# Performance work log

Measured on AMD Instinct MI355X. Metric: run time of the kernel, lower is better.

## Reference

```python
import jax, jax.numpy as jnp
import numpy as np

N_NODES = 30000
N_EDGES = 480000
C = 32          # channel multiplicity of hidden irreps (32x0e + 32x1o)
L = 3           # graph_net_steps
H = 64          # radial MLP hidden width
NB = 8          # num radial basis functions
NS = 5          # num_species
R_MAX = 4.0
AVG_NEIGH = 16.0
N_PATHS = 5     # tensor-product paths per layer


def setup_inputs() -> dict:
    key = jax.random.key(0)
    ks = jax.random.split(key, 16)

    def w(k, shape, fan_in):
        return jax.random.normal(k, shape, jnp.float32) / np.sqrt(fan_in)

    return {
        "vectors": jax.random.normal(ks[0], (N_EDGES, 3), jnp.float32),
        "node_specie": jax.random.randint(ks[1], (N_NODES,), 0, NS),
        "senders": jax.random.randint(ks[2], (N_EDGES,), 0, N_NODES),
        "receivers": jax.random.randint(ks[3], (N_EDGES,), 0, N_NODES),
        "emb": jax.random.normal(ks[4], (NS, C), jnp.float32),
        "w_rad1": w(ks[5], (L, NB, H), NB),
        "w_rad2": w(ks[6], (L, H, H), H),
        "w_rad_out": w(ks[7], (L, H, N_PATHS * C), H),
        "w_lin_s": w(ks[8], (L, 2 * C, 2 * C), 2 * C),
        "w_lin_v": w(ks[9], (L, 3 * C, C), 3 * C),
        "w_sc_s": w(ks[10], (L, NS, C, 2 * C), C),
        "w_sc_v": w(ks[11], (L, NS, C, C), C),
        "w_out1": w(ks[12], (C, 16), C),
        "w_out2": w(ks[13], (16, 1), 16),
    }


def _envelope(x, p=6):
    # smooth polynomial cutoff, = 1 at x=0, = 0 (with zero derivs) at x=1
    u = (1.0 - (p + 1) * (p + 2) / 2 * x**p + p * (p + 2) * x**(p + 1)
         - p * (p + 1) / 2 * x**(p + 2))
    return jnp.where(x < 1.0, u, 0.0)


def _radial_basis(lengths):
    # bessel radial basis [E, NB] with smooth cutoff envelope
    n = jnp.arange(1, NB + 1, dtype=jnp.float32)
    x = lengths / R_MAX
    b = np.sqrt(2.0 / R_MAX) * jnp.sin(n * np.pi * x[:, None]) \
        / jnp.maximum(lengths, 1e-9)[:, None]
    return b * _envelope(x)[:, None]


def reference(vectors, node_specie, senders, receivers, emb, w_rad1, w_rad2,
              w_rad_out, w_lin_s, w_lin_v, w_sc_s, w_sc_v, w_out1, w_out2):
    vectors = vectors / R_MAX                       # as in original __call__
    lengths = jnp.linalg.norm(vectors, axis=-1)
    nhat = vectors / jnp.maximum(lengths, 1e-9)[:, None]   # unit edge vectors
    rb = _radial_basis(lengths)                     # [E, NB]

    s = emb[node_specie]                            # [N, C] scalars (0e)
    v = jnp.zeros((s.shape[0], C, 3), s.dtype)      # [N, C, 3] vectors (1o)

    for l in range(L):
        # radial MLP -> per-path, per-channel edge weights
        h = jax.nn.silu(rb @ w_rad1[l])
        h = jax.nn.silu(h @ w_rad2[l])
        wgt = (h @ w_rad_out[l]).reshape(-1, N_PATHS, C)        # [E, 5, C]

        s_u = s[senders]                                         # [E, C]
        v_u = v[senders]                                         # [E, C, 3]
        ndv = jnp.einsum('ed,ecd->ec', nhat, v_u)                # <n, v>

        # CG tensor-product message paths with spherical harmonics of n
        p0 = wgt[:, 0] * s_u                                     # 0e x Y0 -> 0e
        p1 = wgt[:, 1] * ndv                                     # 1o x Y1 -> 0e
        p2 = wgt[:, 2][:, :, None] * (s_u[:, :, None] * nhat[:, None, :])  # 0e x Y1 -> 1o
        p3 = wgt[:, 3][:, :, None] * v_u                         # 1o x Y0 -> 1o
        p4 = wgt[:, 4][:, :, None] * (nhat[:, None, :] * ndv[:, :, None] - v_u / 3.0)  # 1o x Y2 -> 1o

        agg_s = jax.ops.segment_sum(jnp.concatenate([p0, p1], 1), receivers,
                                    num_segments=N_NODES) / AVG_NEIGH      # [N, 2C]
        agg_v = jax.ops.segment_sum(jnp.concatenate([p2, p3, p4], 1), receivers,
                                    num_segments=N_NODES) / AVG_NEIGH      # [N, 3C, 3]

        sg = agg_s @ w_lin_s[l]                                  # [N, 2C]: C feats + C gates
        vn = jnp.einsum('npd,pc->ncd', agg_v, w_lin_v[l])        # [N, C, 3]
        # self-connection: per-species linear (== tp with species one-hot)
        sg = sg + jnp.einsum('nc,nck->nk', s, w_sc_s[l][node_specie])
        vn = vn + jnp.einsum('ncd,nck->nkd', v, w_sc_v[l][node_specie])

        s_new, gates = jnp.split(sg, 2, axis=1)
        s = jax.nn.silu(s_new)                                   # even activation
        v = jax.nn.silu(gates)[:, :, None] * vn                  # gated 1o

    e = (s @ w_out1) @ w_out2            # Linear '16x0e' -> Linear '0e'
    return e[:, 0]                        # per-node energy [N]
```

## Files before the change

kernel.cpp:

```cpp
#include <hip/hip_runtime.h>
#include <math.h>

#define NNODES 30000
#define NEDGES 480000
#define NC 32
#define NL 3
#define NH 64
#define NBASIS 8
#define NSPEC 5
#define INV_AVG 0.0625f

typedef _Float16 half2v __attribute__((ext_vector_type(2)));
typedef _Float16 half4v __attribute__((ext_vector_type(4)));
typedef _Float16 half8v __attribute__((ext_vector_type(8)));
typedef float    float4v __attribute__((ext_vector_type(4)));
typedef unsigned int uint32;

__device__ __forceinline__ float silu_f(float x) {
    return x / (1.f + __expf(-x));
}
__device__ __forceinline__ float rdlane(float v, int k) {
    return __uint_as_float(__builtin_amdgcn_readlane(__float_as_uint(v), k));
}


__global__ void geom_kernel(const float* __restrict__ vec,
                            float* __restrict__ nhat4,
                            float* __restrict__ rb) {
    int e = blockIdx.x * blockDim.x + threadIdx.x;
    if (e >= NEDGES) return;
    float vx = vec[3*e+0] * 0.25f;
    float vy = vec[3*e+1] * 0.25f;
    float vz = vec[3*e+2] * 0.25f;
    float len = sqrtf(vx*vx + vy*vy + vz*vz);
    float inv = 1.f / fmaxf(len, 1e-9f);
    float4 nh = make_float4(vx*inv, vy*inv, vz*inv, 0.f);
    *(float4*)(nhat4 + (size_t)e*4) = nh;
    float x = len * 0.25f;
    float x3 = x*x*x;
    float x6 = x3*x3;
    float x7 = x6*x;
    float x8 = x7*x;
    float env = (x < 1.f) ? (1.f - 28.f*x6 + 48.f*x7 - 21.f*x8) : 0.f;
    float scale = 0.7071067811865476f * inv * env;
    #pragma unroll
    for (int i = 0; i < NBASIS; ++i) {
        rb[NBASIS*e + i] = scale * sinf((float)(i+1) * 3.14159265358979f * x);
    }
}

__global__ void count_kernel(const int* __restrict__ receivers, int* __restrict__ deg) {
    int e = blockIdx.x * blockDim.x + threadIdx.x;
    if (e >= NEDGES) return;
    atomicAdd(&deg[receivers[e]], 1);
}

__global__ void scan_kernel(const int* __restrict__ deg, int* __restrict__ rowstart) {
    __shared__ int lsum[256];
    __shared__ int loff[256];
    int t = threadIdx.x;
    int lo = t * 118;
    int hi = min(lo + 118, NNODES);
    int s = 0;
    for (int i = lo; i < hi; ++i) s += deg[i];
    lsum[t] = s;
    __syncthreads();
    if (t == 0) {
        int run = 0;
        for (int i = 0; i < 256; ++i) { loff[i] = run; run += lsum[i]; }
    }
    __syncthreads();
    int run = loff[t];
    for (int i = lo; i < hi; ++i) { rowstart[i] = run; run += deg[i]; }
    if (t == 0) rowstart[NNODES] = NEDGES;
}

__global__ void copy_cursor_kernel(const int* __restrict__ rowstart, int* __restrict__ cursor) {
    int i = blockIdx.x * blockDim.x + threadIdx.x;
    if (i < NNODES) cursor[i] = rowstart[i];
}

__global__ void fill_kernel(const int* __restrict__ receivers,
                            int* __restrict__ cursor, int* __restrict__ edge_order) {
    int e = blockIdx.x * blockDim.x + threadIdx.x;
    if (e >= NEDGES) return;
    int pos = atomicAdd(&cursor[receivers[e]], 1);
    edge_order[pos] = e;
}

__global__ void perm_kernel(const int* __restrict__ edge_order,
                            const int* __restrict__ senders,
                            const float* __restrict__ nhat4,
                            float* __restrict__ nh_perm, int* __restrict__ snd_perm) {
    int i = blockIdx.x * blockDim.x + threadIdx.x;
    if (i >= NEDGES) return;
    int e = edge_order[i];
    *(float4*)(nh_perm + (size_t)i*4) = *(const float4*)(nhat4 + (size_t)e*4);
    snd_perm[i] = senders[e];
}

__global__ void prepw_kernel(const float* __restrict__ w1, const float* __restrict__ w2,
                             const float* __restrict__ w3,
                             float* __restrict__ w1t, _Float16* __restrict__ w2f,
                             _Float16* __restrict__ w3f) {
    int t = blockIdx.x * blockDim.x + threadIdx.x;
    if (t < NL * 64 * 8) {
        int l = t / 512, r = t % 512, k = r >> 3, b = r & 7;
        w1t[t] = w1[l * 512 + b * 64 + k];
    }
    int u = t - NL * 64 * 8;
    if (u >= 0 && u < NL * 2 * 4 * 64 * 8) {
        int e = u & 7, lane = (u >> 3) & 63, nt = (u >> 9) & 3, ks = (u >> 11) & 1, l = u >> 12;
        int k = ks * 32 + ((lane >> 4) << 3) + e;
        int col = nt * 16 + (lane & 15);
        w2f[u] = (_Float16)w2[l * 4096 + k * 64 + col];
    }
    int v = t - NL * 64 * 8 - NL * 2 * 4 * 64 * 8;
    if (v >= 0 && v < NL * 2 * 10 * 64 * 8) {
        int q = v / 5120, rem = v % 5120;
        int l = q >> 1, ks = q & 1;
        int nt = rem >> 9, lane = (rem >> 3) & 63, e = rem & 7;
        int k = ks * 32 + ((lane >> 4) << 3) + e;
        int col = nt * 16 + (lane & 15);
        w3f[v] = (_Float16)w3[l * 10240 + k * 160 + col];
    }
}

__global__ void init_kernel(const int* __restrict__ specie,
                            const float* __restrict__ emb,
                            float* __restrict__ s) {
    int t = blockIdx.x * blockDim.x + threadIdx.x;
    if (t >= NNODES * NC) return;
    int n = t >> 5;
    int c = t & 31;
    s[t] = emb[specie[n] * NC + c];
}

__global__ __launch_bounds__(256) void mlpm_kernel(
    const float* __restrict__ rb,
    const int* __restrict__ edge_order,
    const float* __restrict__ w1t,
    const _Float16* __restrict__ w2f,
    const _Float16* __restrict__ w3f,
    _Float16* __restrict__ wgt16)
{
    __shared__ float w1lds[512];
    __shared__ _Float16 tile[4][16][72];

    for (int t = threadIdx.x; t < 512; t += 256) w1lds[t] = w1t[t];
    __syncthreads();

    int lane = threadIdx.x & 63;
    int wid  = threadIdx.x >> 6;
    int c16 = lane & 15;
    int kg  = lane >> 4;
    int ibase = blockIdx.x * 64 + wid * 16;
    int g = blockIdx.x * 4 + wid;

    int e_orig = edge_order[ibase + c16];
    float4 ra4 = *(const float4*)(rb + (size_t)e_orig * 8);
    float4 rb4 = *(const float4*)(rb + (size_t)e_orig * 8 + 4);

    half8v a0, a1;
    #pragma unroll
    for (int e = 0; e < 8; ++e) {
        const float* wr0 = w1lds + (kg * 8 + e) * 8;
        float d0;
        d0 = ra4.x * wr0[0];
        d0 = fmaf(ra4.y, wr0[1], d0);
        d0 = fmaf(ra4.z, wr0[2], d0);
        d0 = fmaf(ra4.w, wr0[3], d0);
        d0 = fmaf(rb4.x, wr0[4], d0);
        d0 = fmaf(rb4.y, wr0[5], d0);
        d0 = fmaf(rb4.z, wr0[6], d0);
        d0 = fmaf(rb4.w, wr0[7], d0);
        a0[e] = (_Float16)silu_f(d0);
        const float* wr1 = w1lds + (32 + kg * 8 + e) * 8;
        float d1;
        d1 = ra4.x * wr1[0];
        d1 = fmaf(ra4.y, wr1[1], d1);
        d1 = fmaf(ra4.z, wr1[2], d1);
        d1 = fmaf(ra4.w, wr1[3], d1);
        d1 = fmaf(rb4.x, wr1[4], d1);
        d1 = fmaf(rb4.y, wr1[5], d1);
        d1 = fmaf(rb4.z, wr1[6], d1);
        d1 = fmaf(rb4.w, wr1[7], d1);
        a1[e] = (_Float16)silu_f(d1);
    }

    _Float16* tw = &tile[wid][0][0];
    float4v zero4 = {0.f, 0.f, 0.f, 0.f};
    #pragma unroll
    for (int nt = 0; nt < 4; ++nt) {
        half8v b0 = *(const half8v*)(w2f + (size_t)(nt) * 512 + lane * 8);
        half8v b1 = *(const half8v*)(w2f + (size_t)(4 + nt) * 512 + lane * 8);
        float4v acc = __builtin_amdgcn_mfma_f32_16x16x32_f16(a0, b0, zero4, 0, 0, 0);
        acc = __builtin_amdgcn_mfma_f32_16x16x32_f16(a1, b1, acc, 0, 0, 0);
        #pragma unroll
        for (int r = 0; r < 4; ++r)
            tw[(kg * 4 + r) * 72 + nt * 16 + c16] = (_Float16)silu_f(acc[r]);
    }

    half8v a2 = *(const half8v*)(tw + c16 * 72 + kg * 8);
    half8v a3 = *(const half8v*)(tw + c16 * 72 + 32 + kg * 8);

    _Float16* out = wgt16 + (size_t)g * 2560 + lane * 4;
    #pragma unroll
    for (int nt = 0; nt < 10; ++nt) {
        half8v b0 = *(const half8v*)(w3f + (size_t)(nt) * 512 + lane * 8);
        half8v b1 = *(const half8v*)(w3f + (size_t)(10 + nt) * 512 + lane * 8);
        float4v acc = __builtin_amdgcn_mfma_f32_16x16x32_f16(a2, b0, zero4, 0, 0, 0);
        acc = __builtin_amdgcn_mfma_f32_16x16x32_f16(a3, b1, acc, 0, 0, 0);
        half4v o;
        o[0] = (_Float16)acc[0];
        o[1] = (_Float16)acc[1];
        o[2] = (_Float16)acc[2];
        o[3] = (_Float16)acc[3];
        *(half4v*)(out + nt * 256) = o;
    }
}

__global__ __launch_bounds__(512) void gather_tp_kernel(
    const _Float16* __restrict__ wgt16,
    const float* __restrict__ nh_perm,
    const int* __restrict__ snd_perm,
    const int* __restrict__ rowstart, const int* __restrict__ deg,
    const float* __restrict__ s_in, const float* __restrict__ v_in,
    float* __restrict__ agg_s,
    float* __restrict__ agg_v)
{
    int lane = threadIdx.x & 63;
    int wid  = threadIdx.x >> 6;
    int n = blockIdx.x * 8 + wid;
    if (n >= NNODES) return;

    int c = lane & 31;
    int half = lane >> 5;

    int c16g = c & 15;
    int off0 = (2 * half + (c >> 4)) * 256 + c16g * 4;
    int off1 = (4 + 2 * half + (c >> 4)) * 256 + c16g * 4;
    int off2 = (8 + (c >> 4)) * 256 + c16g * 4;

    float accS = 0.f;
    float aVa0 = 0.f, aVa1 = 0.f, aVa2 = 0.f;
    float aVb0 = 0.f, aVb1 = 0.f, aVb2 = 0.f;

    int start = rowstart[n];
    int cnt   = deg[n];

    int snd_n = 0;
    float4 nh_n = make_float4(0.f, 0.f, 0.f, 0.f);
    if (cnt > 0) {
        snd_n = snd_perm[start];
        nh_n  = *(const float4*)(nh_perm + (size_t)start * 4);
    }

    for (int i = 0; i < cnt; ++i) {
        int idx = start + i;
        int snd = snd_n;
        float4 nh = nh_n;
        size_t base_e = (size_t)(idx >> 4) * 2560 + ((idx & 15) >> 2) * 64 + (idx & 3);

        float d0  = (float)wgt16[base_e + off0];
        float d1  = (float)wgt16[base_e + off1];
        float d2f = (float)wgt16[base_e + off2];

        if (i + 1 < cnt) {
            snd_n = snd_perm[idx + 1];
            nh_n  = *(const float4*)(nh_perm + (size_t)(idx + 1) * 4);
        }

        float su = s_in[(size_t)snd * NC + c];
        float v0 = v_in[(size_t)snd * 96 + c];
        float v1 = v_in[(size_t)snd * 96 + 32 + c];
        float v2 = v_in[(size_t)snd * 96 + 64 + c];
        float ndv = nh.x * v0;
        ndv = fmaf(nh.y, v1, ndv);
        ndv = fmaf(nh.z, v2, ndv);

        float sSel = half ? ndv : su;
        accS = fmaf(d0, sSel, accS);
        float scale = half ? d1 : d1 * su;
        float f0 = half ? v0 : nh.x;
        float f1 = half ? v1 : nh.y;
        float f2 = half ? v2 : nh.z;
        aVa0 = fmaf(scale, f0, aVa0);
        aVa1 = fmaf(scale, f1, aVa1);
        aVa2 = fmaf(scale, f2, aVa2);
        float m4 = half ? 0.f : d2f;
        aVb0 = fmaf(m4, fmaf(nh.x, ndv, -v0 * (1.f / 3.f)), aVb0);
        aVb1 = fmaf(m4, fmaf(nh.y, ndv, -v1 * (1.f / 3.f)), aVb1);
        aVb2 = fmaf(m4, fmaf(nh.z, ndv, -v2 * (1.f / 3.f)), aVb2);
    }

    agg_s[(size_t)n * 64 + lane] = accS;
    float* av = agg_v + (size_t)n * 288;
    if (half == 0) {
        av[c * 3 + 0] = aVa0; av[c * 3 + 1] = aVa1; av[c * 3 + 2] = aVa2;
        av[(64 + c) * 3 + 0] = aVb0; av[(64 + c) * 3 + 1] = aVb1; av[(64 + c) * 3 + 2] = aVb2;
    } else {
        av[(32 + c) * 3 + 0] = aVa0; av[(32 + c) * 3 + 1] = aVa1; av[(32 + c) * 3 + 2] = aVa2;
    }
}

__global__ __launch_bounds__(512) void gather_kernel(
    const float* __restrict__ rb, const float* __restrict__ nhat4,
    const int* __restrict__ senders, const int* __restrict__ edge_order,
    const int* __restrict__ rowstart, const int* __restrict__ deg,
    const float* __restrict__ s_in, const float* __restrict__ v_in,
    const float* __restrict__ w1, const float* __restrict__ w2, const float* __restrict__ w3,
    float* __restrict__ agg_s, float* __restrict__ agg_v)
{
    __shared__ float sW2[NH * NH];
    __shared__ float sW3[NH * 160];
    for (int i = threadIdx.x; i < NH * NH;  i += 512) sW2[i] = w2[i];
    for (int i = threadIdx.x; i < NH * 160; i += 512) sW3[i] = w3[i];
    __syncthreads();
    int lane = threadIdx.x & 63;
    int wid  = threadIdx.x >> 6;
    int n = blockIdx.x * 8 + wid;
    if (n >= NNODES) return;
    int c = lane & 31;
    int half = lane >> 5;
    float w1r[8];
    #pragma unroll
    for (int b = 0; b < 8; ++b) w1r[b] = w1[b * NH + lane];
    float accS = 0.f;
    float aVa0 = 0.f, aVa1 = 0.f, aVa2 = 0.f;
    float aVb0 = 0.f, aVb1 = 0.f, aVb2 = 0.f;
    int start = rowstart[n];
    int cnt   = deg[n];
    for (int i = 0; i < cnt; ++i) {
        int e   = edge_order[start + i];
        int snd = senders[e];
        float4 nh  = *(const float4*)(nhat4 + (size_t)e * 4);
        float4 rba = *(const float4*)(rb + (size_t)e * 8);
        float4 rbb = *(const float4*)(rb + (size_t)e * 8 + 4);
        float h1v;
        h1v = rba.x * w1r[0];
        h1v = fmaf(rba.y, w1r[1], h1v);
        h1v = fmaf(rba.z, w1r[2], h1v);
        h1v = fmaf(rba.w, w1r[3], h1v);
        h1v = fmaf(rbb.x, w1r[4], h1v);
        h1v = fmaf(rbb.y, w1r[5], h1v);
        h1v = fmaf(rbb.z, w1r[6], h1v);
        h1v = fmaf(rbb.w, w1r[7], h1v);
        h1v = silu_f(h1v);
        float a0 = 0.f, a1 = 0.f;
        #pragma unroll
        for (int k = 0; k < NH; k += 2) {
            a0 = fmaf(rdlane(h1v, k),     sW2[k * NH + lane],       a0);
            a1 = fmaf(rdlane(h1v, k + 1), sW2[(k + 1) * NH + lane], a1);
        }
        float h2v = silu_f(a0 + a1);
        float d0a = 0.f, d0b = 0.f, d1a = 0.f, d1b = 0.f, d2a = 0.f, d2b = 0.f;
        #pragma unroll
        for (int k = 0; k < NH; k += 2) {
            float hA = rdlane(h2v, k);
            float hB = rdlane(h2v, k + 1);
            d0a = fmaf(hA, sW3[k * 160 + lane],            d0a);
            d1a = fmaf(hA, sW3[k * 160 + 64 + lane],       d1a);
            d2a = fmaf(hA, sW3[k * 160 + 128 + c],         d2a);
            d0b = fmaf(hB, sW3[(k + 1) * 160 + lane],      d0b);
            d1b = fmaf(hB, sW3[(k + 1) * 160 + 64 + lane], d1b);
            d2b = fmaf(hB, sW3[(k + 1) * 160 + 128 + c],   d2b);
        }
        float d0 = d0a + d0b;
        float d1 = d1a + d1b;
        float d2 = d2a + d2b;
        float su = s_in[(size_t)snd * NC + c];
        float v0 = v_in[(size_t)snd * 96 + c];
        float v1 = v_in[(size_t)snd * 96 + 32 + c];
        float v2 = v_in[(size_t)snd * 96 + 64 + c];
        float ndv = nh.x * v0;
        ndv = fmaf(nh.y, v1, ndv);
        ndv = fmaf(nh.z, v2, ndv);
        float sSel = half ? ndv : su;
        accS = fmaf(d0, sSel, accS);
        float scale = half ? d1 : d1 * su;
        float f0 = half ? v0 : nh.x;
        float f1 = half ? v1 : nh.y;
        float f2 = half ? v2 : nh.z;
        aVa0 = fmaf(scale, f0, aVa0);
        aVa1 = fmaf(scale, f1, aVa1);
        aVa2 = fmaf(scale, f2, aVa2);
        float m4 = half ? 0.f : d2;
        aVb0 = fmaf(m4, fmaf(nh.x, ndv, -v0 * (1.f / 3.f)), aVb0);
        aVb1 = fmaf(m4, fmaf(nh.y, ndv, -v1 * (1.f / 3.f)), aVb1);
        aVb2 = fmaf(m4, fmaf(nh.z, ndv, -v2 * (1.f / 3.f)), aVb2);
    }
    agg_s[(size_t)n * 64 + lane] = accS;
    float* av = agg_v + (size_t)n * 288;
    if (half == 0) {
        av[c * 3 + 0] = aVa0; av[c * 3 + 1] = aVa1; av[c * 3 + 2] = aVa2;
        av[(64 + c) * 3 + 0] = aVb0; av[(64 + c) * 3 + 1] = aVb1; av[(64 + c) * 3 + 2] = aVb2;
    } else {
        av[(32 + c) * 3 + 0] = aVa0; av[(32 + c) * 3 + 1] = aVa1; av[(32 + c) * 3 + 2] = aVa2;
    }
}

__global__ __launch_bounds__(256) void node_kernel(
    const int* __restrict__ specie,
    const float* __restrict__ agg_s, const float* __restrict__ agg_v,
    const float* __restrict__ s_in,  const float* __restrict__ v_in,
    const float* __restrict__ wls,
    const float* __restrict__ wlv,
    const float* __restrict__ wscs,
    const float* __restrict__ wscv,
    float* __restrict__ s_out, float* __restrict__ v_out)
{
    __shared__ float sAV[4][288];
    __shared__ float sVO[4][96];

    int lane = threadIdx.x & 63;
    int wid  = threadIdx.x >> 6;
    int n = blockIdx.x * 4 + wid;
    if (n >= NNODES) return;
    int sp = specie[n];

    const float* av = agg_v + (size_t)n * 288;
    sAV[wid][lane]       = av[lane];
    sAV[wid][64 + lane]  = av[64 + lane];
    sAV[wid][128 + lane] = av[128 + lane];
    sAV[wid][192 + lane] = av[192 + lane];
    if (lane < 32) sAV[wid][256 + lane] = av[256 + lane];
    const float* vo = v_in + (size_t)n * 96;
    if (lane < 32) {
        sVO[wid][lane]      = vo[lane];
        sVO[wid][32 + lane] = vo[32 + lane];
        sVO[wid][64 + lane] = vo[64 + lane];
    }

    float asv = agg_s[(size_t)n * 64 + lane];
    float sv  = s_in[(size_t)n * 32 + (lane & 31)];

    __syncthreads();

    float sg = 0.f;
    #pragma unroll
    for (int j = 0; j < 64; ++j)
        sg = fmaf(rdlane(asv, j), wls[j * 64 + lane], sg);
    sg *= INV_AVG;
    const float* ws = wscs + (size_t)sp * 32 * 64;
    #pragma unroll
    for (int j = 0; j < 32; ++j)
        sg = fmaf(rdlane(sv, j), ws[j * 64 + lane], sg);
    float act  = silu_f(sg);
    float gate = __shfl(act, (lane & 31) + 32);

    int c = lane & 31;
    int h = lane >> 5;
    float vn1 = 0.f, vn2 = 0.f;
    #pragma unroll
    for (int p = 0; p < 96; ++p) {
        float w = wlv[p * 32 + c];
        vn1 = fmaf(sAV[wid][3 * p + h], w, vn1);
        vn2 = fmaf(sAV[wid][3 * p + 2], w, vn2);
    }
    vn1 *= INV_AVG; vn2 *= INV_AVG;
    const float* wv = wscv + (size_t)sp * 32 * 32;
    #pragma unroll
    for (int j = 0; j < 32; ++j) {
        float w = wv[j * 32 + c];
        vn1 = fmaf(sVO[wid][h * 32 + j], w, vn1);
        vn2 = fmaf(sVO[wid][64 + j],     w, vn2);
    }

    if (lane < 32) s_out[(size_t)n * 32 + lane] = act;
    v_out[(size_t)n * 96 + h * 32 + c] = gate * vn1;
    if (h == 0) v_out[(size_t)n * 96 + 64 + c] = gate * vn2;
}

__global__ void out_kernel(const float* __restrict__ s,
                           const float* __restrict__ w1,
                           const float* __restrict__ w2,
                           float* __restrict__ out) {
    int n = blockIdx.x * blockDim.x + threadIdx.x;
    if (n >= NNODES) return;
    float sv[NC];
    #pragma unroll
    for (int c = 0; c < NC; ++c) sv[c] = s[(size_t)n * NC + c];
    float e = 0.f;
    #pragma unroll
    for (int j = 0; j < 16; ++j) {
        float tj = 0.f;
        #pragma unroll
        for (int c = 0; c < NC; ++c) tj += sv[c] * w1[c * 16 + j];
        e += tj * w2[j];
    }
    out[n] = e;
}

extern "C" void kernel_launch(void* const* d_in, const int* in_sizes, int n_in,
                              void* d_out, int out_size, void* d_ws, size_t ws_size,
                              hipStream_t stream) {
    const float* vectors   = (const float*)d_in[0];
    const int*   specie    = (const int*)  d_in[1];
    const int*   senders   = (const int*)  d_in[2];
    const int*   receivers = (const int*)  d_in[3];
    const float* emb       = (const float*)d_in[4];
    const float* w_rad1    = (const float*)d_in[5];
    const float* w_rad2    = (const float*)d_in[6];
    const float* w_rad_out = (const float*)d_in[7];
    const float* w_lin_s   = (const float*)d_in[8];
    const float* w_lin_v   = (const float*)d_in[9];
    const float* w_sc_s    = (const float*)d_in[10];
    const float* w_sc_v    = (const float*)d_in[11];
    const float* w_out1    = (const float*)d_in[12];
    const float* w_out2    = (const float*)d_in[13];

    char* base = (char*)d_ws;
    size_t off = 0;
    auto alloc = [&](size_t bytes) { char* q = base + off; off += (bytes + 255) & ~(size_t)255; return q; };

    float* nhat4 = (float*)alloc((size_t)NEDGES * 4 * 4);
    float* rb    = (float*)alloc((size_t)NEDGES * 8 * 4);
    float* s_a   = (float*)alloc((size_t)NNODES * NC * 4);
    float* v_a   = (float*)alloc((size_t)NNODES * NC * 3 * 4);
    float* s_b   = (float*)alloc((size_t)NNODES * NC * 4);
    float* v_b   = (float*)alloc((size_t)NNODES * NC * 3 * 4);
    float* aggs  = (float*)alloc((size_t)NNODES * 2 * NC * 4);
    float* aggv  = (float*)alloc((size_t)NNODES * 3 * NC * 3 * 4);
    int* deg        = (int*)alloc((size_t)NNODES * 4);
    int* rowstart   = (int*)alloc((size_t)(NNODES + 4) * 4);
    int* cursor     = (int*)alloc((size_t)NNODES * 4);
    int* edge_order = (int*)alloc((size_t)NEDGES * 4);
    float*    nh_perm  = (float*)alloc((size_t)NEDGES * 4 * 4);
    int*      snd_perm = (int*)alloc((size_t)NEDGES * 4);
    float*    w1t      = (float*)alloc((size_t)NL * 64 * 8 * 4);
    _Float16* w2f      = (_Float16*)alloc((size_t)NL * 2 * 4 * 64 * 8 * 2);
    _Float16* w3f      = (_Float16*)alloc((size_t)NL * 2 * 10 * 64 * 8 * 2);
    _Float16* wgt16    = (_Float16*)alloc((size_t)NEDGES * 160 * 2);
    bool big = (off <= ws_size);

    geom_kernel<<<(NEDGES + 255) / 256, 256, 0, stream>>>(vectors, nhat4, rb);
    (void)hipMemsetAsync(deg, 0, NNODES * sizeof(int), stream);
    count_kernel<<<(NEDGES + 255) / 256, 256, 0, stream>>>(receivers, deg);
    scan_kernel<<<1, 256, 0, stream>>>(deg, rowstart);
    copy_cursor_kernel<<<(NNODES + 255) / 256, 256, 0, stream>>>(rowstart, cursor);
    fill_kernel<<<(NEDGES + 255) / 256, 256, 0, stream>>>(receivers, cursor, edge_order);
    if (big) {
        perm_kernel<<<(NEDGES + 255) / 256, 256, 0, stream>>>(
            edge_order, senders, nhat4, nh_perm, snd_perm);
        int prep_n = NL * 64 * 8 + NL * 2 * 4 * 64 * 8 + NL * 2 * 10 * 64 * 8;
        prepw_kernel<<<(prep_n + 255) / 256, 256, 0, stream>>>(
            w_rad1, w_rad2, w_rad_out, w1t, w2f, w3f);
    }

    init_kernel<<<(NNODES * NC + 255) / 256, 256, 0, stream>>>(specie, emb, s_a);
    (void)hipMemsetAsync(v_a, 0, (size_t)NNODES * NC * 3 * sizeof(float), stream);

    float* si = s_a; float* vi = v_a; float* so = s_b; float* vo = v_b;
    for (int l = 0; l < NL; ++l) {
        if (big) {
            mlpm_kernel<<<NEDGES / 64, 256, 0, stream>>>(
                rb, edge_order,
                w1t + (size_t)l * 512,
                w2f + (size_t)l * 4096,
                w3f + (size_t)l * 10240,
                wgt16);
            gather_tp_kernel<<<NNODES / 8, 512, 0, stream>>>(
                wgt16, nh_perm, snd_perm, rowstart, deg, si, vi, aggs, aggv);
        } else {
            gather_kernel<<<NNODES / 8, 512, 0, stream>>>(
                rb, nhat4, senders, edge_order, rowstart, deg, si, vi,
                w_rad1 + (size_t)l * NBASIS * NH,
                w_rad2 + (size_t)l * NH * NH,
                w_rad_out + (size_t)l * NH * 160,
                aggs, aggv);
        }
        node_kernel<<<(NNODES + 3) / 4, 256, 0, stream>>>(
            specie, aggs, aggv, si, vi,
            w_lin_s + (size_t)l * 64 * 64,
            w_lin_v + (size_t)l * 96 * 32,
            w_sc_s + (size_t)l * NSPEC * NC * 64,
            w_sc_v + (size_t)l * NSPEC * NC * NC,
            so, vo);
        float* ts = si; si = so; so = ts;
        float* tv = vi; vi = vo; vo = tv;
    }

    out_kernel<<<(NNODES + 255) / 256, 256, 0, stream>>>(si, w_out1, w_out2, (float*)d_out);
}
```

Baseline: 744.2 us.

## Fuse node linear update into gather tensor-product kernel

Fold the per-node linear layers, species self-connection and gated activation into the gather kernel. Each wavefront keeps its aggregated scalars in registers (shared via readlane) and its vector aggregates in LDS. This removes the separate node_kernel launch and the global round trip of agg_s/agg_v per layer. In exchange, the gather kernel's register pressure and per-wave serial work go up, and weights are read from global/cache per wave.

```diff
diff --git a/kernel.cpp b/kernel.cpp
--- a/kernel.cpp
+++ b/kernel.cpp
@@ -220,15 +220,22 @@
     }
 }
 
-__global__ __launch_bounds__(512) void gather_tp_kernel(
+__global__ __launch_bounds__(512) void gather_node_kernel(
     const _Float16* __restrict__ wgt16,
     const float* __restrict__ nh_perm,
     const int* __restrict__ snd_perm,
     const int* __restrict__ rowstart, const int* __restrict__ deg,
+    const int* __restrict__ specie,
     const float* __restrict__ s_in, const float* __restrict__ v_in,
-    float* __restrict__ agg_s,
-    float* __restrict__ agg_v)
+    const float* __restrict__ wls,
+    const float* __restrict__ wlv,
+    const float* __restrict__ wscs,
+    const float* __restrict__ wscv,
+    float* __restrict__ s_out, float* __restrict__ v_out)
 {
+    __shared__ float sAV[8][288];
+    __shared__ float sVO[8][96];
+
     int lane = threadIdx.x & 63;
     int wid  = threadIdx.x >> 6;
     int n = blockIdx.x * 8 + wid;
@@ -294,14 +301,50 @@
         aVb2 = fmaf(m4, fmaf(nh.z, ndv, -v2 * (1.f / 3.f)), aVb2);
     }
 
-    agg_s[(size_t)n * 64 + lane] = accS;
-    float* av = agg_v + (size_t)n * 288;
     if (half == 0) {
-        av[c * 3 + 0] = aVa0; av[c * 3 + 1] = aVa1; av[c * 3 + 2] = aVa2;
-        av[(64 + c) * 3 + 0] = aVb0; av[(64 + c) * 3 + 1] = aVb1; av[(64 + c) * 3 + 2] = aVb2;
+        sAV[wid][c * 3 + 0] = aVa0; sAV[wid][c * 3 + 1] = aVa1; sAV[wid][c * 3 + 2] = aVa2;
+        sAV[wid][(64 + c) * 3 + 0] = aVb0; sAV[wid][(64 + c) * 3 + 1] = aVb1; sAV[wid][(64 + c) * 3 + 2] = aVb2;
     } else {
-        av[(32 + c) * 3 + 0] = aVa0; av[(32 + c) * 3 + 1] = aVa1; av[(32 + c) * 3 + 2] = aVa2;
-    }
+        sAV[wid][(32 + c) * 3 + 0] = aVa0; sAV[wid][(32 + c) * 3 + 1] = aVa1; sAV[wid][(32 + c) * 3 + 2] = aVa2;
+    }
+    const float* vo = v_in + (size_t)n * 96;
+    sVO[wid][lane] = vo[lane];
+    if (lane < 32) sVO[wid][64 + lane] = vo[64 + lane];
+
+    int sp = specie[n];
+    float sv = s_in[(size_t)n * 32 + c];
+
+    float sg = 0.f;
+    #pragma unroll
+    for (int j = 0; j < 64; ++j)
+        sg = fmaf(rdlane(accS, j), wls[j * 64 + lane], sg);
+    sg *= INV_AVG;
+    const float* ws = wscs + (size_t)sp * 32 * 64;
+    #pragma unroll
+    for (int j = 0; j < 32; ++j)
+        sg = fmaf(rdlane(sv, j), ws[j * 64 + lane], sg);
+    float act  = silu_f(sg);
+    float gate = __shfl(act, c + 32);
+
+    float vn1 = 0.f, vn2 = 0.f;
+    #pragma unroll
+    for (int p = 0; p < 96; ++p) {
+        float w = wlv[p * 32 + c];
+        vn1 = fmaf(sAV[wid][3 * p + half], w, vn1);
+        vn2 = fmaf(sAV[wid][3 * p + 2],    w, vn2);
+    }
+    vn1 *= INV_AVG; vn2 *= INV_AVG;
+    const float* wv = wscv + (size_t)sp * 32 * 32;
+    #pragma unroll
+    for (int j = 0; j < 32; ++j) {
+        float w = wv[j * 32 + c];
+        vn1 = fmaf(sVO[wid][half * 32 + j], w, vn1);
+        vn2 = fmaf(sVO[wid][64 + j],        w, vn2);
+    }
+
+    if (lane < 32) s_out[(size_t)n * 32 + lane] = act;
+    v_out[(size_t)n * 96 + half * 32 + c] = gate * vn1;
+    if (half == 0) v_out[(size_t)n * 96 + 64 + c] = gate * vn2;
 }
 
 __global__ __launch_bounds__(512) void gather_kernel(
@@ -560,8 +603,13 @@
                 w2f + (size_t)l * 4096,
                 w3f + (size_t)l * 10240,
                 wgt16);
-            gather_tp_kernel<<<NNODES / 8, 512, 0, stream>>>(
-                wgt16, nh_perm, snd_perm, rowstart, deg, si, vi, aggs, aggv);
+            gather_node_kernel<<<(NNODES + 7) / 8, 512, 0, stream>>>(
+                wgt16, nh_perm, snd_perm, rowstart, deg, specie, si, vi,
+                w_lin_s + (size_t)l * 64 * 64,
+                w_lin_v + (size_t)l * 96 * 32,
+                w_sc_s + (size_t)l * NSPEC * NC * 64,
+                w_sc_v + (size_t)l * NSPEC * NC * NC,
+                so, vo);
         } else {
             gather_kernel<<<NNODES / 8, 512, 0, stream>>>(
                 rb, nhat4, senders, edge_order, rowstart, deg, si, vi,
@@ -569,14 +617,14 @@
                 w_rad2 + (size_t)l * NH * NH,
                 w_rad_out + (size_t)l * NH * 160,
                 aggs, aggv);
+            node_kernel<<<(NNODES + 3) / 4, 256, 0, stream>>>(
+                specie, aggs, aggv, si, vi,
+                w_lin_s + (size_t)l * 64 * 64,
+                w_lin_v + (size_t)l * 96 * 32,
+                w_sc_s + (size_t)l * NSPEC * NC * 64,
+                w_sc_v + (size_t)l * NSPEC * NC * NC,
+                so, vo);
         }
-        node_kernel<<<(NNODES + 3) / 4, 256, 0, stream>>>(
-            specie, aggs, aggv, si, vi,
-            w_lin_s + (size_t)l * 64 * 64,
-            w_lin_v + (size_t)l * 96 * 32,
-            w_sc_s + (size_t)l * NSPEC * NC * 64,
-            w_sc_v + (size_t)l * NSPEC * NC * NC,
-            so, vo);
         float* ts = si; si = so; so = ts;
         float* tv = vi; vi = vo; vo = tv;
     }
```

New measurement: 912.6 us. 22.6% more time.

## Fuse geometry with edge permutation and store node features in fp16

Applied to the files above, without the earlier changes.

The geometry kernel is merged with the permutation step. The fill kernel now records each edge's sorted position, and geometry writes nhat, sender and the radial basis straight into sorted order. This removes the separate perm kernel, the edge_order indirection in the MLP kernel and one extra pass over the edges. Node scalar and vector features are also stored as fp16 to halve the bytes of the random sender gathers, at some cost in precision. The fallback path for a small workspace is dropped, so the function now returns early when the workspace is too small.

```diff
diff --git a/kernel.cpp b/kernel.cpp
--- a/kernel.cpp
+++ b/kernel.cpp
@@ -23,31 +23,6 @@
     return __uint_as_float(__builtin_amdgcn_readlane(__float_as_uint(v), k));
 }
 
-
-__global__ void geom_kernel(const float* __restrict__ vec,
-                            float* __restrict__ nhat4,
-                            float* __restrict__ rb) {
-    int e = blockIdx.x * blockDim.x + threadIdx.x;
-    if (e >= NEDGES) return;
-    float vx = vec[3*e+0] * 0.25f;
-    float vy = vec[3*e+1] * 0.25f;
-    float vz = vec[3*e+2] * 0.25f;
-    float len = sqrtf(vx*vx + vy*vy + vz*vz);
-    float inv = 1.f / fmaxf(len, 1e-9f);
-    float4 nh = make_float4(vx*inv, vy*inv, vz*inv, 0.f);
-    *(float4*)(nhat4 + (size_t)e*4) = nh;
-    float x = len * 0.25f;
-    float x3 = x*x*x;
-    float x6 = x3*x3;
-    float x7 = x6*x;
-    float x8 = x7*x;
-    float env = (x < 1.f) ? (1.f - 28.f*x6 + 48.f*x7 - 21.f*x8) : 0.f;
-    float scale = 0.7071067811865476f * inv * env;
-    #pragma unroll
-    for (int i = 0; i < NBASIS; ++i) {
-        rb[NBASIS*e + i] = scale * sinf((float)(i+1) * 3.14159265358979f * x);
-    }
-}
 
 __global__ void count_kernel(const int* __restrict__ receivers, int* __restrict__ deg) {
     int e = blockIdx.x * blockDim.x + threadIdx.x;
@@ -81,22 +56,41 @@
 }
 
 __global__ void fill_kernel(const int* __restrict__ receivers,
-                            int* __restrict__ cursor, int* __restrict__ edge_order) {
+                            int* __restrict__ cursor, int* __restrict__ epos) {
     int e = blockIdx.x * blockDim.x + threadIdx.x;
     if (e >= NEDGES) return;
-    int pos = atomicAdd(&cursor[receivers[e]], 1);
-    edge_order[pos] = e;
-}
-
-__global__ void perm_kernel(const int* __restrict__ edge_order,
-                            const int* __restrict__ senders,
-                            const float* __restrict__ nhat4,
-                            float* __restrict__ nh_perm, int* __restrict__ snd_perm) {
-    int i = blockIdx.x * blockDim.x + threadIdx.x;
-    if (i >= NEDGES) return;
-    int e = edge_order[i];
-    *(float4*)(nh_perm + (size_t)i*4) = *(const float4*)(nhat4 + (size_t)e*4);
-    snd_perm[i] = senders[e];
+    epos[e] = atomicAdd(&cursor[receivers[e]], 1);
+}
+
+__global__ void geom_perm_kernel(const float* __restrict__ vec,
+                                 const int* __restrict__ senders,
+                                 const int* __restrict__ epos,
+                                 float* __restrict__ nh_perm,
+                                 int* __restrict__ snd_perm,
+                                 float* __restrict__ rb_perm) {
+    int e = blockIdx.x * blockDim.x + threadIdx.x;
+    if (e >= NEDGES) return;
+    float vx = vec[3*e+0] * 0.25f;
+    float vy = vec[3*e+1] * 0.25f;
+    float vz = vec[3*e+2] * 0.25f;
+    float len = sqrtf(vx*vx + vy*vy + vz*vz);
+    float inv = 1.f / fmaxf(len, 1e-9f);
+    int p = epos[e];
+    *(float4*)(nh_perm + (size_t)p*4) = make_float4(vx*inv, vy*inv, vz*inv, 0.f);
+    snd_perm[p] = senders[e];
+    float x = len * 0.25f;
+    float x3 = x*x*x;
+    float x6 = x3*x3;
+    float x7 = x6*x;
+    float x8 = x7*x;
+    float env = (x < 1.f) ? (1.f - 28.f*x6 + 48.f*x7 - 21.f*x8) : 0.f;
+    float scale = 0.7071067811865476f * inv * env;
+    float rbv[8];
+    #pragma unroll
+    for (int i = 0; i < NBASIS; ++i)
+        rbv[i] = scale * sinf((float)(i+1) * 3.14159265358979f * x);
+    *(float4*)(rb_perm + (size_t)p*8)     = make_float4(rbv[0], rbv[1], rbv[2], rbv[3]);
+    *(float4*)(rb_perm + (size_t)p*8 + 4) = make_float4(rbv[4], rbv[5], rbv[6], rbv[7]);
 }
 
 __global__ void prepw_kernel(const float* __restrict__ w1, const float* __restrict__ w2,
@@ -128,17 +122,16 @@
 
 __global__ void init_kernel(const int* __restrict__ specie,
                             const float* __restrict__ emb,
-                            float* __restrict__ s) {
+                            _Float16* __restrict__ s) {
     int t = blockIdx.x * blockDim.x + threadIdx.x;
     if (t >= NNODES * NC) return;
     int n = t >> 5;
     int c = t & 31;
-    s[t] = emb[specie[n] * NC + c];
+    s[t] = (_Float16)emb[specie[n] * NC + c];
 }
 
 __global__ __launch_bounds__(256) void mlpm_kernel(
-    const float* __restrict__ rb,
-    const int* __restrict__ edge_order,
+    const float* __restrict__ rb_perm,
     const float* __restrict__ w1t,
     const _Float16* __restrict__ w2f,
     const _Float16* __restrict__ w3f,
@@ -157,9 +150,8 @@
     int ibase = blockIdx.x * 64 + wid * 16;
     int g = blockIdx.x * 4 + wid;
 
-    int e_orig = edge_order[ibase + c16];
-    float4 ra4 = *(const float4*)(rb + (size_t)e_orig * 8);
-    float4 rb4 = *(const float4*)(rb + (size_t)e_orig * 8 + 4);
+    float4 ra4 = *(const float4*)(rb_perm + (size_t)(ibase + c16) * 8);
+    float4 rb4 = *(const float4*)(rb_perm + (size_t)(ibase + c16) * 8 + 4);
 
     half8v a0, a1;
     #pragma unroll
@@ -225,7 +217,7 @@
     const float* __restrict__ nh_perm,
     const int* __restrict__ snd_perm,
     const int* __restrict__ rowstart, const int* __restrict__ deg,
-    const float* __restrict__ s_in, const float* __restrict__ v_in,
+    const _Float16* __restrict__ s_in, const _Float16* __restrict__ v_in,
     float* __restrict__ agg_s,
     float* __restrict__ agg_v)
 {
@@ -271,10 +263,10 @@
             nh_n  = *(const float4*)(nh_perm + (size_t)(idx + 1) * 4);
         }
 
-        float su = s_in[(size_t)snd * NC + c];
-        float v0 = v_in[(size_t)snd * 96 + c];
-        float v1 = v_in[(size_t)snd * 96 + 32 + c];
-        float v2 = v_in[(size_t)snd * 96 + 64 + c];
+        float su = (float)s_in[(size_t)snd * NC + c];
+        float v0 = (float)v_in[(size_t)snd * 96 + c];
+        float v1 = (float)v_in[(size_t)snd * 96 + 32 + c];
+        float v2 = (float)v_in[(size_t)snd * 96 + 64 + c];
         float ndv = nh.x * v0;
         ndv = fmaf(nh.y, v1, ndv);
         ndv = fmaf(nh.z, v2, ndv);
@@ -304,111 +296,15 @@
     }
 }
 
-__global__ __launch_bounds__(512) void gather_kernel(
-    const float* __restrict__ rb, const float* __restrict__ nhat4,
-    const int* __restrict__ senders, const int* __restrict__ edge_order,
-    const int* __restrict__ rowstart, const int* __restrict__ deg,
-    const float* __restrict__ s_in, const float* __restrict__ v_in,
-    const float* __restrict__ w1, const float* __restrict__ w2, const float* __restrict__ w3,
-    float* __restrict__ agg_s, float* __restrict__ agg_v)
-{
-    __shared__ float sW2[NH * NH];
-    __shared__ float sW3[NH * 160];
-    for (int i = threadIdx.x; i < NH * NH;  i += 512) sW2[i] = w2[i];
-    for (int i = threadIdx.x; i < NH * 160; i += 512) sW3[i] = w3[i];
-    __syncthreads();
-    int lane = threadIdx.x & 63;
-    int wid  = threadIdx.x >> 6;
-    int n = blockIdx.x * 8 + wid;
-    if (n >= NNODES) return;
-    int c = lane & 31;
-    int half = lane >> 5;
-    float w1r[8];
-    #pragma unroll
-    for (int b = 0; b < 8; ++b) w1r[b] = w1[b * NH + lane];
-    float accS = 0.f;
-    float aVa0 = 0.f, aVa1 = 0.f, aVa2 = 0.f;
-    float aVb0 = 0.f, aVb1 = 0.f, aVb2 = 0.f;
-    int start = rowstart[n];
-    int cnt   = deg[n];
-    for (int i = 0; i < cnt; ++i) {
-        int e   = edge_order[start + i];
-        int snd = senders[e];
-        float4 nh  = *(const float4*)(nhat4 + (size_t)e * 4);
-        float4 rba = *(const float4*)(rb + (size_t)e * 8);
-        float4 rbb = *(const float4*)(rb + (size_t)e * 8 + 4);
-        float h1v;
-        h1v = rba.x * w1r[0];
-        h1v = fmaf(rba.y, w1r[1], h1v);
-        h1v = fmaf(rba.z, w1r[2], h1v);
-        h1v = fmaf(rba.w, w1r[3], h1v);
-        h1v = fmaf(rbb.x, w1r[4], h1v);
-        h1v = fmaf(rbb.y, w1r[5], h1v);
-        h1v = fmaf(rbb.z, w1r[6], h1v);
-        h1v = fmaf(rbb.w, w1r[7], h1v);
-        h1v = silu_f(h1v);
-        float a0 = 0.f, a1 = 0.f;
-        #pragma unroll
-        for (int k = 0; k < NH; k += 2) {
-            a0 = fmaf(rdlane(h1v, k),     sW2[k * NH + lane],       a0);
-            a1 = fmaf(rdlane(h1v, k + 1), sW2[(k + 1) * NH + lane], a1);
-        }
-        float h2v = silu_f(a0 + a1);
-        float d0a = 0.f, d0b = 0.f, d1a = 0.f, d1b = 0.f, d2a = 0.f, d2b = 0.f;
-        #pragma unroll
-        for (int k = 0; k < NH; k += 2) {
-            float hA = rdlane(h2v, k);
-            float hB = rdlane(h2v, k + 1);
-            d0a = fmaf(hA, sW3[k * 160 + lane],            d0a);
-            d1a = fmaf(hA, sW3[k * 160 + 64 + lane],       d1a);
-            d2a = fmaf(hA, sW3[k * 160 + 128 + c],         d2a);
-            d0b = fmaf(hB, sW3[(k + 1) * 160 + lane],      d0b);
-            d1b = fmaf(hB, sW3[(k + 1) * 160 + 64 + lane], d1b);
-            d2b = fmaf(hB, sW3[(k + 1) * 160 + 128 + c],   d2b);
-        }
-        float d0 = d0a + d0b;
-        float d1 = d1a + d1b;
-        float d2 = d2a + d2b;
-        float su = s_in[(size_t)snd * NC + c];
-        float v0 = v_in[(size_t)snd * 96 + c];
-        float v1 = v_in[(size_t)snd * 96 + 32 + c];
-        float v2 = v_in[(size_t)snd * 96 + 64 + c];
-        float ndv = nh.x * v0;
-        ndv = fmaf(nh.y, v1, ndv);
-        ndv = fmaf(nh.z, v2, ndv);
-        float sSel = half ? ndv : su;
-        accS = fmaf(d0, sSel, accS);
-        float scale = half ? d1 : d1 * su;
-        float f0 = half ? v0 : nh.x;
-        float f1 = half ? v1 : nh.y;
-        float f2 = half ? v2 : nh.z;
-        aVa0 = fmaf(scale, f0, aVa0);
-        aVa1 = fmaf(scale, f1, aVa1);
-        aVa2 = fmaf(scale, f2, aVa2);
-        float m4 = half ? 0.f : d2;
-        aVb0 = fmaf(m4, fmaf(nh.x, ndv, -v0 * (1.f / 3.f)), aVb0);
-        aVb1 = fmaf(m4, fmaf(nh.y, ndv, -v1 * (1.f / 3.f)), aVb1);
-        aVb2 = fmaf(m4, fmaf(nh.z, ndv, -v2 * (1.f / 3.f)), aVb2);
-    }
-    agg_s[(size_t)n * 64 + lane] = accS;
-    float* av = agg_v + (size_t)n * 288;
-    if (half == 0) {
-        av[c * 3 + 0] = aVa0; av[c * 3 + 1] = aVa1; av[c * 3 + 2] = aVa2;
-        av[(64 + c) * 3 + 0] = aVb0; av[(64 + c) * 3 + 1] = aVb1; av[(64 + c) * 3 + 2] = aVb2;
-    } else {
-        av[(32 + c) * 3 + 0] = aVa0; av[(32 + c) * 3 + 1] = aVa1; av[(32 + c) * 3 + 2] = aVa2;
-    }
-}
-
 __global__ __launch_bounds__(256) void node_kernel(
     const int* __restrict__ specie,
     const float* __restrict__ agg_s, const float* __restrict__ agg_v,
-    const float* __restrict__ s_in,  const float* __restrict__ v_in,
+    const _Float16* __restrict__ s_in,  const _Float16* __restrict__ v_in,
     const float* __restrict__ wls,
     const float* __restrict__ wlv,
     const float* __restrict__ wscs,
     const float* __restrict__ wscv,
-    float* __restrict__ s_out, float* __restrict__ v_out)
+    _Float16* __restrict__ s_out, _Float16* __restrict__ v_out)
 {
     __shared__ float sAV[4][288];
     __shared__ float sVO[4][96];
@@ -425,15 +321,15 @@
     sAV[wid][128 + lane] = av[128 + lane];
     sAV[wid][192 + lane] = av[192 + lane];
     if (lane < 32) sAV[wid][256 + lane] = av[256 + lane];
-    const float* vo = v_in + (size_t)n * 96;
+    const _Float16* vo = v_in + (size_t)n * 96;
     if (lane < 32) {
-        sVO[wid][lane]      = vo[lane];
-        sVO[wid][32 + lane] = vo[32 + lane];
-        sVO[wid][64 + lane] = vo[64 + lane];
+        sVO[wid][lane]      = (float)vo[lane];
+        sVO[wid][32 + lane] = (float)vo[32 + lane];
+        sVO[wid][64 + lane] = (float)vo[64 + lane];
     }
 
     float asv = agg_s[(size_t)n * 64 + lane];
-    float sv  = s_in[(size_t)n * 32 + (lane & 31)];
+    float sv  = (float)s_in[(size_t)n * 32 + (lane & 31)];
 
     __syncthreads();
 
@@ -467,12 +363,12 @@
         vn2 = fmaf(sVO[wid][64 + j],     w, vn2);
     }
 
-    if (lane < 32) s_out[(size_t)n * 32 + lane] = act;
-    v_out[(size_t)n * 96 + h * 32 + c] = gate * vn1;
-    if (h == 0) v_out[(size_t)n * 96 + 64 + c] = gate * vn2;
-}
-
-__global__ void out_kernel(const float* __restrict__ s,
+    if (lane < 32) s_out[(size_t)n * 32 + lane] = (_Float16)act;
+    v_out[(size_t)n * 96 + h * 32 + c] = (_Float16)(gate * vn1);
+    if (h == 0) v_out[(size_t)n * 96 + 64 + c] = (_Float16)(gate * vn2);
+}
+
+__global__ void out_kernel(const _Float16* __restrict__ s,
                            const float* __restrict__ w1,
                            const float* __restrict__ w2,
                            float* __restrict__ out) {
@@ -480,7 +376,7 @@
     if (n >= NNODES) return;
     float sv[NC];
     #pragma unroll
-    for (int c = 0; c < NC; ++c) sv[c] = s[(size_t)n * NC + c];
+    for (int c = 0; c < NC; ++c) sv[c] = (float)s[(size_t)n * NC + c];
     float e = 0.f;
     #pragma unroll
     for (int j = 0; j < 16; ++j) {
@@ -514,62 +410,49 @@
     size_t off = 0;
     auto alloc = [&](size_t bytes) { char* q = base + off; off += (bytes + 255) & ~(size_t)255; return q; };
 
-    float* nhat4 = (float*)alloc((size_t)NEDGES * 4 * 4);
-    float* rb    = (float*)alloc((size_t)NEDGES * 8 * 4);
-    float* s_a   = (float*)alloc((size_t)NNODES * NC * 4);
-    float* v_a   = (float*)alloc((size_t)NNODES * NC * 3 * 4);
-    float* s_b   = (float*)alloc((size_t)NNODES * NC * 4);
-    float* v_b   = (float*)alloc((size_t)NNODES * NC * 3 * 4);
-    float* aggs  = (float*)alloc((size_t)NNODES * 2 * NC * 4);
-    float* aggv  = (float*)alloc((size_t)NNODES * 3 * NC * 3 * 4);
+    float*    nh_perm  = (float*)alloc((size_t)NEDGES * 4 * 4);
+    float*    rb_perm  = (float*)alloc((size_t)NEDGES * 8 * 4);
+    int*      snd_perm = (int*)alloc((size_t)NEDGES * 4);
+    int*      epos     = (int*)alloc((size_t)NEDGES * 4);
+    _Float16* s_a      = (_Float16*)alloc((size_t)NNODES * NC * 2);
+    _Float16* v_a      = (_Float16*)alloc((size_t)NNODES * NC * 3 * 2);
+    _Float16* s_b      = (_Float16*)alloc((size_t)NNODES * NC * 2);
+    _Float16* v_b      = (_Float16*)alloc((size_t)NNODES * NC * 3 * 2);
+    float*    aggs     = (float*)alloc((size_t)NNODES * 2 * NC * 4);
+    float*    aggv     = (float*)alloc((size_t)NNODES * 3 * NC * 3 * 4);
     int* deg        = (int*)alloc((size_t)NNODES * 4);
     int* rowstart   = (int*)alloc((size_t)(NNODES + 4) * 4);
     int* cursor     = (int*)alloc((size_t)NNODES * 4);
-    int* edge_order = (int*)alloc((size_t)NEDGES * 4);
-    float*    nh_perm  = (float*)alloc((size_t)NEDGES * 4 * 4);
-    int*      snd_perm = (int*)alloc((size_t)NEDGES * 4);
     float*    w1t      = (float*)alloc((size_t)NL * 64 * 8 * 4);
     _Float16* w2f      = (_Float16*)alloc((size_t)NL * 2 * 4 * 64 * 8 * 2);
     _Float16* w3f      = (_Float16*)alloc((size_t)NL * 2 * 10 * 64 * 8 * 2);
     _Float16* wgt16    = (_Float16*)alloc((size_t)NEDGES * 160 * 2);
-    bool big = (off <= ws_size);
-
-    geom_kernel<<<(NEDGES + 255) / 256, 256, 0, stream>>>(vectors, nhat4, rb);
+    if (off > ws_size) return;
+
     (void)hipMemsetAsync(deg, 0, NNODES * sizeof(int), stream);
     count_kernel<<<(NEDGES + 255) / 256, 256, 0, stream>>>(receivers, deg);
     scan_kernel<<<1, 256, 0, stream>>>(deg, rowstart);
     copy_cursor_kernel<<<(NNODES + 255) / 256, 256, 0, stream>>>(rowstart, cursor);
-    fill_kernel<<<(NEDGES + 255) / 256, 256, 0, stream>>>(receivers, cursor, edge_order);
-    if (big) {
-        perm_kernel<<<(NEDGES + 255) / 256, 256, 0, stream>>>(
-            edge_order, senders, nhat4, nh_perm, snd_perm);
-        int prep_n = NL * 64 * 8 + NL * 2 * 4 * 64 * 8 + NL * 2 * 10 * 64 * 8;
-        prepw_kernel<<<(prep_n + 255) / 256, 256, 0, stream>>>(
-            w_rad1, w_rad2, w_rad_out, w1t, w2f, w3f);
-    }
+    fill_kernel<<<(NEDGES + 255) / 256, 256, 0, stream>>>(receivers, cursor, epos);
+    geom_perm_kernel<<<(NEDGES + 255) / 256, 256, 0, stream>>>(
+        vectors, senders, epos, nh_perm, snd_perm, rb_perm);
+    int prep_n = NL * 64 * 8 + NL * 2 * 4 * 64 * 8 + NL * 2 * 10 * 64 * 8;
+    prepw_kernel<<<(prep_n + 255) / 256, 256, 0, stream>>>(
+        w_rad1, w_rad2, w_rad_out, w1t, w2f, w3f);
 
     init_kernel<<<(NNODES * NC + 255) / 256, 256, 0, stream>>>(specie, emb, s_a);
-    (void)hipMemsetAsync(v_a, 0, (size_t)NNODES * NC * 3 * sizeof(float), stream);
-
-    float* si = s_a; float* vi = v_a; float* so = s_b; float* vo = v_b;
+    (void)hipMemsetAsync(v_a, 0, (size_t)NNODES * NC * 3 * 2, stream);
+
+    _Float16* si = s_a; _Float16* vi = v_a; _Float16* so = s_b; _Float16* vo = v_b;
     for (int l = 0; l < NL; ++l) {
-        if (big) {
-            mlpm_kernel<<<NEDGES / 64, 256, 0, stream>>>(
-                rb, edge_order,
-                w1t + (size_t)l * 512,
-                w2f + (size_t)l * 4096,
-                w3f + (size_t)l * 10240,
-                wgt16);
-            gather_tp_kernel<<<NNODES / 8, 512, 0, stream>>>(
-                wgt16, nh_perm, snd_perm, rowstart, deg, si, vi, aggs, aggv);
-        } else {
-            gather_kernel<<<NNODES / 8, 512, 0, stream>>>(
-                rb, nhat4, senders, edge_order, rowstart, deg, si, vi,
-                w_rad1 + (size_t)l * NBASIS * NH,
-                w_rad2 + (size_t)l * NH * NH,
-                w_rad_out + (size_t)l * NH * 160,
-                aggs, aggv);
-        }
+        mlpm_kernel<<<NEDGES / 64, 256, 0, stream>>>(
+            rb_perm,
+            w1t + (size_t)l * 512,
+            w2f + (size_t)l * 4096,
+            w3f + (size_t)l * 10240,
+            wgt16);
+        gather_tp_kernel<<<(NNODES + 7) / 8, 512, 0, stream>>>(
+            wgt16, nh_perm, snd_perm, rowstart, deg, si, vi, aggs, aggv);
         node_kernel<<<(NNODES + 3) / 4, 256, 0, stream>>>(
             specie, aggs, aggv, si, vi,
             w_lin_s + (size_t)l * 64 * 64,
@@ -577,8 +460,8 @@
             w_sc_s + (size_t)l * NSPEC * NC * 64,
             w_sc_v + (size_t)l * NSPEC * NC * NC,
             so, vo);
-        float* ts = si; si = so; so = ts;
-        float* tv = vi; vi = vo; vo = tv;
+        _Float16* ts = si; si = so; so = ts;
+        _Float16* tv = vi; vi = vo; vo = tv;
     }
 
     out_kernel<<<(NNODES + 255) / 256, 256, 0, stream>>>(si, w_out1, w_out2, (float*)d_out);
```

Measured after the change: 751.2 us. Within noise of the previous version (+0.9%).
